# Kernel tuning notes

Measured on AMD Instinct MI355X. Metric: run time of the kernel, lower is better.

The kernel has to match this reference:

```python
import jax, jax.numpy as jnp
import numpy as np

# Model constants (match init_kwargs)
H, P, N, G, NL, K = 32, 64, 128, 1, 15, 4   # heads, head_dim, state, groups, lambda levels, conv width
HID, T, BATCH = 1024, 1024, 1
INTER = H * P                    # 2048
CONV_DIM = INTER + 2 * G * N     # 2304
PROJ = INTER + CONV_DIM + H * (NL + 1)  # 4864
EPS = 1e-5


def _level_matrix(t_len: int) -> np.ndarray:
    """Fenwick-tree level assignment: for query t, prefix [0,t] splits into
    power-of-two segments from binary expansion of t+1; segment of length 2^l -> level l."""
    lm = np.zeros((t_len, t_len), dtype=np.int32)
    for t in range(t_len):
        n = t + 1
        while n > 0:
            lb = n & (-n)
            lm[t, n - lb:n] = lb.bit_length() - 1
            n -= lb
    return lm


def setup_inputs() -> dict:
    key = jax.random.key(0)
    ks = jax.random.split(key, 4)
    return {
        "hidden_states": jax.random.normal(ks[0], (BATCH, T, HID), jnp.float32),
        "in_proj_w": jax.random.normal(ks[1], (PROJ, HID), jnp.float32) / np.sqrt(HID).astype(np.float32),
        "in_proj_b": jnp.zeros((PROJ,), jnp.float32),
        "conv_w": jax.random.normal(ks[2], (CONV_DIM, K), jnp.float32) / np.sqrt(K).astype(np.float32),
        "dt_bias": jnp.ones((H,), jnp.float32),
        "A_log": jnp.log(jnp.arange(1, H + 1, dtype=jnp.float32)),
        "L_param": jnp.ones((H, NL), jnp.float32),
        "D": jnp.ones((H,), jnp.float32),
        "rmsnorm_w": jnp.ones((INTER,), jnp.float32),
        "out_proj_w": jax.random.normal(ks[3], (HID, INTER), jnp.float32) / np.sqrt(INTER).astype(np.float32),
        "out_proj_b": jnp.zeros((HID,), jnp.float32),
        "level_mat": jnp.asarray(_level_matrix(T)),  # (T,T) int32, data-independent
    }


def reference(hidden_states, in_proj_w, in_proj_b, conv_w, dt_bias, A_log,
              L_param, D, rmsnorm_w, out_proj_w, out_proj_b, level_mat):
    b, t, _ = hidden_states.shape
    # in_proj and split: [z | xBC | dt | dl]
    zxbcdtdl = hidden_states @ in_proj_w.T + in_proj_b
    z, xBC, dt, dl = jnp.split(zxbcdtdl, [INTER, INTER + CONV_DIM, INTER + CONV_DIM + H], axis=-1)
    # depthwise causal conv1d (width K) + SiLU
    xp = jnp.pad(xBC, ((0, 0), (K - 1, 0), (0, 0)))
    conv = sum(xp[:, w:w + t, :] * conv_w[:, w] for w in range(K))
    xBC = jax.nn.silu(conv)
    x, Bm, Cm = jnp.split(xBC, [INTER, INTER + G * N], axis=-1)
    x = x.reshape(b, t, H, P)          # v pre-scale
    Bm = Bm.reshape(b, t, G, N)        # keys
    Cm = Cm.reshape(b, t, G, N)        # queries
    dl = dl.reshape(b, t, H, NL)
    # D residual uses unscaled x (matches hmamba_chunk_scan_combined ordering)
    D_res = x * D[None, None, :, None]
    dt = jax.nn.softplus(dt + dt_bias)            # (b,t,H)
    v = x * dt[..., None]                          # (b,t,H,P)
    A = -jnp.exp(A_log)                            # (H,)
    g = A * dt                                     # (b,t,H), per-token log-decay (<=0)
    Ls = jax.nn.softplus(L_param * dl)             # (b,t,H,NL) per-token level scales
    # cumulative log-decay; decay(t,s) = exp(cg_t - cg_s), s<=t
    cg = jnp.cumsum(g, axis=1).transpose(0, 2, 1)  # (b,H,t)
    mask = jnp.tril(jnp.ones((t, t), bool))
    logdecay = jnp.where(mask, cg[:, :, :, None] - cg[:, :, None, :], -jnp.inf)
    decay = jnp.exp(logdecay)                      # (b,H,t,s)
    # hierarchical level scale H[t,s] = Ls[b,t,h, level(t,s)]
    Hmat = jnp.take_along_axis(Ls.transpose(0, 2, 1, 3), level_mat[None, None, :, :], axis=-1)  # (b,H,t,s)
    scores = jnp.einsum('btgn,bsgn->bgts', Cm, Bm)  # (b,G,t,s), G=1 broadcasts over heads
    att = scores * decay * Hmat                     # (b,H,t,s), masked via decay=0
    y = jnp.einsum('bhts,bshp->bthp', att, v) + D_res
    y = y.reshape(b, t, INTER)
    # gated RMSNorm with norm_before_gate=False: normalize(y * silu(z)) * w
    yg = y * jax.nn.silu(z)
    y = yg * jax.lax.rsqrt(jnp.mean(yg * yg, axis=-1, keepdims=True) + EPS) * rmsnorm_w
    return y @ out_proj_w.T + out_proj_b
```

## Files before the change

kernel.cpp:

```cpp
#include <hip/hip_runtime.h>
#include <hip/hip_bf16.h>
#include <math.h>

#define T_LEN 1024
#define HID 1024
#define NHEAD 32
#define HDIM 64
#define NSTATE 128
#define NLVL 15
#define KCONV 4
#define INTER 2048
#define CONV_DIM 2304
#define PROJ 4864
#define EPS 1e-5f

typedef __attribute__((ext_vector_type(8))) _Float16 half8;
typedef __attribute__((ext_vector_type(4))) float float4v;
typedef unsigned short ushort_t;

__device__ __forceinline__ float softplus_f(float x) {
  return fmaxf(x, 0.f) + log1pf(expf(-fabsf(x)));
}
__device__ __forceinline__ float silu_f(float x) {
  return x / (1.f + expf(-x));
}
__device__ __forceinline__ ushort_t f2h(float f) {
  union { _Float16 h; ushort_t u; } v;
  v.h = (_Float16)f;
  return v.u;
}
__device__ __forceinline__ void gload_lds16(const void* g, void* l) {
  __builtin_amdgcn_global_load_lds(
      (const __attribute__((address_space(1))) void*)g,
      (__attribute__((address_space(3))) void*)l, 16, 0, 0);
}

#define N4_HS  (T_LEN * HID / 4)
#define N4_WI  (PROJ * HID / 4)
#define N4_WO  (HID * INTER / 4)
__global__ __launch_bounds__(256) void prep_f16(
    const float* __restrict__ hs, const float* __restrict__ wi,
    const float* __restrict__ wo, ushort_t* __restrict__ hsb,
    ushort_t* __restrict__ wib, ushort_t* __restrict__ wob) {
  int i = blockIdx.x * 256 + threadIdx.x;
  const float* src; ushort_t* dst; int j;
  if (i < N4_HS)              { src = hs; dst = hsb; j = i; }
  else if (i < N4_HS + N4_WI) { src = wi; dst = wib; j = i - N4_HS; }
  else                        { src = wo; dst = wob; j = i - N4_HS - N4_WI; }
  float4 v = reinterpret_cast<const float4*>(src)[j];
  union { ushort_t u[4]; unsigned long long ll; } o;
  o.u[0] = f2h(v.x); o.u[1] = f2h(v.y); o.u[2] = f2h(v.z); o.u[3] = f2h(v.w);
  reinterpret_cast<unsigned long long*>(dst)[j] = o.ll;
}

__global__ __launch_bounds__(256) void gemm_f16_sk(
    const ushort_t* __restrict__ A, const ushort_t* __restrict__ B,
    float* __restrict__ Cpart, int M, int N, int K, int Kc) {
  __shared__ ushort_t As[2][128][32];
  __shared__ ushort_t Bs[2][128][32];
  const int tid = threadIdx.x;
  const int w = tid >> 6, L = tid & 63;
  const int n0 = blockIdx.x * 128, m0 = blockIdx.y * 128;
  const int kbeg = blockIdx.z * Kc;
  float* __restrict__ C = Cpart + (size_t)blockIdx.z * M * N;
  const int mq = (w & 1) * 64, nq = (w >> 1) * 64;
  const int srow = (L >> 2);
  const int sch = (L & 3) * 8;

  float4v acc[4][4];
#pragma unroll
  for (int i = 0; i < 4; ++i)
#pragma unroll
    for (int j = 0; j < 4; ++j) acc[i][j] = (float4v){0.f, 0.f, 0.f, 0.f};

  const int niter = Kc / 32;
  {
    const int kk = kbeg;
#pragma unroll
    for (int j = 0; j < 2; ++j) {
      int r0 = 16 * (w * 2 + j);
      gload_lds16(A + (size_t)(m0 + r0 + srow) * K + kk + sch, &As[0][r0][0]);
      gload_lds16(B + (size_t)(n0 + r0 + srow) * K + kk + sch, &Bs[0][r0][0]);
    }
  }
  for (int it = 0; it < niter; ++it) {
    __syncthreads();
    if (it + 1 < niter) {
      const int kk = kbeg + (it + 1) * 32;
      const int nb = (it + 1) & 1;
#pragma unroll
      for (int j = 0; j < 2; ++j) {
        int r0 = 16 * (w * 2 + j);
        gload_lds16(A + (size_t)(m0 + r0 + srow) * K + kk + sch, &As[nb][r0][0]);
        gload_lds16(B + (size_t)(n0 + r0 + srow) * K + kk + sch, &Bs[nb][r0][0]);
      }
    }
    const int cb = it & 1;
    half8 af[4], bf[4];
#pragma unroll
    for (int t = 0; t < 4; ++t) {
      af[t] = *reinterpret_cast<const half8*>(&As[cb][mq + t * 16 + (L & 15)][(L >> 4) * 8]);
      bf[t] = *reinterpret_cast<const half8*>(&Bs[cb][nq + t * 16 + (L & 15)][(L >> 4) * 8]);
    }
#pragma unroll
    for (int mt = 0; mt < 4; ++mt)
#pragma unroll
      for (int nt = 0; nt < 4; ++nt)
        acc[mt][nt] = __builtin_amdgcn_mfma_f32_16x16x32_f16(af[mt], bf[nt], acc[mt][nt], 0, 0, 0);
  }
  const int qrow = (L >> 4) * 4;
#pragma unroll
  for (int mt = 0; mt < 4; ++mt) {
#pragma unroll
    for (int nt = 0; nt < 4; ++nt) {
      int col = n0 + nq + nt * 16 + (L & 15);
#pragma unroll
      for (int r = 0; r < 4; ++r) {
        int row = m0 + mq + mt * 16 + qrow + r;
        C[(size_t)row * N + col] = acc[mt][nt][r];
      }
    }
  }
}

__global__ __launch_bounds__(256) void reduce_out4(const float* __restrict__ p,
                                                   const float* __restrict__ bias,
                                                   float* __restrict__ out, int MN) {
  int i = blockIdx.x * 256 + threadIdx.x;
  if (i * 4 >= MN) return;
  float4 a = reinterpret_cast<const float4*>(p)[i];
  float4 b = reinterpret_cast<const float4*>(p + MN)[i];
  float4 c = reinterpret_cast<const float4*>(p + 2 * (size_t)MN)[i];
  float4 d = reinterpret_cast<const float4*>(p + 3 * (size_t)MN)[i];
  int col = (i * 4) & (HID - 1);
  float4 bv = *reinterpret_cast<const float4*>(bias + col);
  float4 o;
  o.x = a.x + b.x + c.x + d.x + bv.x;
  o.y = a.y + b.y + c.y + d.y + bv.y;
  o.z = a.z + b.z + c.z + d.z + bv.z;
  o.w = a.w + b.w + c.w + d.w + bv.w;
  reinterpret_cast<float4*>(out)[i] = o;
}

__global__ __launch_bounds__(512) void pointwise_dt(
    const float* __restrict__ zx0, const float* __restrict__ zx1,
    const float* __restrict__ in_b, const float* __restrict__ dt_bias,
    const float* __restrict__ A_log, const float* __restrict__ L_param,
    float* __restrict__ dtbuf, float* __restrict__ gT,
    float* __restrict__ Lsbuf) {
  const int t = blockIdx.x;
  const int j = threadIdx.x;
  const size_t ro = (size_t)t * PROJ;
  if (j < NHEAD * NLVL) {
    int c = INTER + CONV_DIM + NHEAD + j;
    float x = L_param[j] * (zx0[ro + c] + zx1[ro + c] + in_b[c]);
    Lsbuf[(size_t)t * (NHEAD * NLVL) + j] = softplus_f(x);
  } else {
    int h = j - NHEAD * NLVL;
    int c = INTER + CONV_DIM + h;
    float x = zx0[ro + c] + zx1[ro + c] + in_b[c] + dt_bias[h];
    float dt = softplus_f(x);
    dtbuf[t * NHEAD + h] = dt;
    gT[h * T_LEN + t] = -expf(A_log[h]) * dt;
  }
}

__global__ __launch_bounds__(64) void scan_g(const float* __restrict__ gT,
                                             double* __restrict__ cgd) {
  const int h = blockIdx.x, l = threadIdx.x;
  const float* gr = gT + (size_t)h * T_LEN + l * 16;
  double pre[16];
  double acc = 0.0;
#pragma unroll
  for (int i = 0; i < 16; ++i) { acc += (double)gr[i]; pre[i] = acc; }
  double s = acc;
#pragma unroll
  for (int off = 1; off < 64; off <<= 1) {
    double o = __shfl_up(s, off, 64);
    if (l >= off) s += o;
  }
  const double base = s - acc;
  double* cr = cgd + (size_t)h * T_LEN + l * 16;
#pragma unroll
  for (int i = 0; i < 16; ++i) cr[i] = base + pre[i];
}

__global__ __launch_bounds__(256) void conv_fused(
    const float* __restrict__ zx0, const float* __restrict__ zx1,
    const float* __restrict__ in_b, const float* __restrict__ conv_w,
    const float* __restrict__ dtbuf, const float* __restrict__ Dp,
    ushort_t* __restrict__ vt, float* __restrict__ ybuf,
    ushort_t* __restrict__ Bb, ushort_t* __restrict__ Cb) {
  __shared__ ushort_t Vl[64][68];
  __shared__ float dtl[64];
  const int tq = blockIdx.x, cy = blockIdx.y;
  const int t0 = tq * 64;
  const int tid = threadIdx.x;
  const int lane = tid & 63, g = tid >> 6;
  const bool vpath = (cy < 32);
  const int ccol = vpath ? cy * 64 + lane : INTER + (cy - 32) * 64 + lane;
  const int zcol = INTER + ccol;
  float cw[KCONV];
#pragma unroll
  for (int w = 0; w < KCONV; ++w) cw[w] = conv_w[ccol * KCONV + w];
  const float bc = in_b[zcol];
  if (vpath && tid < 64) dtl[tid] = dtbuf[(t0 + tid) * NHEAD + cy];
  const float Dh = vpath ? Dp[cy] : 0.f;

  float xv[19];
#pragma unroll
  for (int i = 0; i < 19; ++i) {
    int tt = t0 + g * 16 - 3 + i;
    if (tt >= 0) {
      size_t o = (size_t)tt * PROJ + zcol;
      xv[i] = zx0[o] + zx1[o] + bc;
    } else xv[i] = 0.f;
  }
  __syncthreads();
#pragma unroll
  for (int i = 0; i < 16; ++i) {
    float acc = xv[i] * cw[0] + xv[i + 1] * cw[1] + xv[i + 2] * cw[2] + xv[i + 3] * cw[3];
    float sil = silu_f(acc);
    int tl = g * 16 + i;
    int t = t0 + tl;
    if (vpath) {
      ushort_t vh = f2h(sil * dtl[tl]);
      Vl[tl][lane] = vh;
      ybuf[(size_t)t * INTER + cy * 64 + lane] = sil * Dh;
    } else if (ccol < INTER + NSTATE) {
      Bb[t * NSTATE + (ccol - INTER)] = f2h(sil);
    } else {
      Cb[t * NSTATE + (ccol - INTER - NSTATE)] = f2h(sil);
    }
  }
  if (vpath) {
    __syncthreads();
#pragma unroll
    for (int rep = 0; rep < 2; ++rep) {
      int u = tid + 256 * rep;
      int p = u >> 3, t8 = (u & 7) * 8;
      union { ushort_t u16[8]; half8 h; } o;
#pragma unroll
      for (int j = 0; j < 8; ++j) o.u16[j] = Vl[t8 + j][p];
      *reinterpret_cast<half8*>(vt + (size_t)(cy * 64 + p) * T_LEN + t0 + t8) = o.h;
    }
  }
}

__global__ __launch_bounds__(256) void attn_mfma(
    const ushort_t* __restrict__ Bb, const ushort_t* __restrict__ Cb,
    const ushort_t* __restrict__ vt, const double* __restrict__ cgd,
    const float* __restrict__ Lsb, float* __restrict__ ybuf) {
  __shared__ ushort_t Bl[64][136];
  __shared__ ushort_t Vtl[64][72];
  __shared__ ushort_t Sl[64][72];
  __shared__ float Lsl[64][16];
  __shared__ float cgq[64];
  __shared__ float cgs[64];

  const int item = blockIdx.x;
  const int h = item / 40;
  const int rem = item - h * 40;
  int qt, j;
  if (rem < 4)        { qt = rem;                 j = 0; }
  else if (rem < 12)  { qt = 4 + (rem - 4) / 2;   j = (rem - 4) % 2; }
  else if (rem < 24)  { qt = 8 + (rem - 12) / 3;  j = (rem - 12) % 3; }
  else                { qt = 12 + (rem - 24) / 4; j = (rem - 24) % 4; }

  const int tid = threadIdx.x;
  const int w = tid >> 6, L = tid & 63;
  const int tq0 = qt * 64;
  const double* cgh = cgd + (size_t)h * T_LEN;
  const double base = cgh[tq0];

  for (int i = tid; i < 64 * NLVL; i += 256) {
    int r = i / NLVL, l = i - r * NLVL;
    Lsl[r][l] = Lsb[(size_t)(tq0 + r) * (NHEAD * NLVL) + h * NLVL + l];
  }
  if (tid < 64) cgq[tid] = (float)(cgh[tq0 + tid] - base);

  half8 cfrag[4];
  {
    const ushort_t* cr = Cb + (size_t)(tq0 + w * 16 + (L & 15)) * NSTATE + (L >> 4) * 8;
#pragma unroll
    for (int ks = 0; ks < 4; ++ks)
      cfrag[ks] = *reinterpret_cast<const half8*>(cr + ks * 32);
  }
  float4v yac[4];
#pragma unroll
  for (int i = 0; i < 4; ++i) yac[i] = (float4v){0.f, 0.f, 0.f, 0.f};

  const int qrow = w * 16 + ((L >> 4) << 2);

  const int st0 = 4 * j;
  const int st1 = min(4 * j + 4, qt + 1);
  for (int st = st0; st < st1; ++st) {
    const int ts0 = st * 64;
    __syncthreads();
#pragma unroll
    for (int i = 0; i < 4; ++i) {
      int u = tid + 256 * i;
      int row = u >> 4, kb = (u & 15) * 8;
      *reinterpret_cast<half8*>(&Bl[row][kb]) =
          *reinterpret_cast<const half8*>(Bb + (size_t)(ts0 + row) * NSTATE + kb);
    }
#pragma unroll
    for (int i = 0; i < 2; ++i) {
      int u = tid + 256 * i;
      int p = u >> 3, sc = (u & 7) * 8;
      *reinterpret_cast<half8*>(&Vtl[p][sc]) =
          *reinterpret_cast<const half8*>(vt + (size_t)(h * HDIM + p) * T_LEN + ts0 + sc);
    }
    if (tid < 64) cgs[tid] = (float)(cgh[ts0 + tid] - base);
    __syncthreads();

    float4v sac[4];
#pragma unroll
    for (int nt = 0; nt < 4; ++nt) sac[nt] = (float4v){0.f, 0.f, 0.f, 0.f};
#pragma unroll
    for (int ks = 0; ks < 4; ++ks) {
#pragma unroll
      for (int nt = 0; nt < 4; ++nt) {
        half8 bfrag = *reinterpret_cast<const half8*>(&Bl[nt * 16 + (L & 15)][ks * 32 + (L >> 4) * 8]);
        sac[nt] = __builtin_amdgcn_mfma_f32_16x16x32_f16(cfrag[ks], bfrag, sac[nt], 0, 0, 0);
      }
    }
#pragma unroll
    for (int nt = 0; nt < 4; ++nt) {
      int s = nt * 16 + (L & 15);
      int sg = ts0 + s;
      float cs = cgs[s];
#pragma unroll
      for (int r = 0; r < 4; ++r) {
        int q = qrow + r;
        int tg = tq0 + q;
        float val = 0.f;
        if (sg <= tg) {
          int lvl = 31 - __clz((unsigned)(sg ^ (tg + 1)));
          val = sac[nt][r] * __expf(cgq[q] - cs) * Lsl[q][lvl];
        }
        Sl[q][s] = f2h(val);
      }
    }
    __builtin_amdgcn_s_waitcnt(0);
#pragma unroll
    for (int ks = 0; ks < 2; ++ks) {
      half8 af = *reinterpret_cast<const half8*>(&Sl[w * 16 + (L & 15)][ks * 32 + (L >> 4) * 8]);
#pragma unroll
      for (int pt = 0; pt < 4; ++pt) {
        half8 bfv = *reinterpret_cast<const half8*>(&Vtl[pt * 16 + (L & 15)][ks * 32 + (L >> 4) * 8]);
        yac[pt] = __builtin_amdgcn_mfma_f32_16x16x32_f16(af, bfv, yac[pt], 0, 0, 0);
      }
    }
  }
#pragma unroll
  for (int pt = 0; pt < 4; ++pt) {
    int p = pt * 16 + (L & 15);
#pragma unroll
    for (int r = 0; r < 4; ++r) {
      int q = qrow + r;
      atomicAdd(ybuf + (size_t)(tq0 + q) * INTER + h * HDIM + p, yac[pt][r]);
    }
  }
}

__global__ __launch_bounds__(256) void rmsnorm_gate(
    const float* __restrict__ ybuf, const float* __restrict__ zx0,
    const float* __restrict__ zx1, const float* __restrict__ in_b,
    const float* __restrict__ w, ushort_t* __restrict__ yhf) {
  __shared__ float red[4];
  const int t = blockIdx.x, tid = threadIdx.x;
  const size_t ro = (size_t)t * PROJ;
  const float* yrow = ybuf + (size_t)t * INTER;
  float yg[8];
  float ss = 0.f;
#pragma unroll
  for (int i = 0; i < 8; ++i) {
    int c = tid + 256 * i;
    float z = zx0[ro + c] + zx1[ro + c] + in_b[c];
    float g = yrow[c] * silu_f(z);
    yg[i] = g;
    ss += g * g;
  }
#pragma unroll
  for (int off = 32; off; off >>= 1) ss += __shfl_down(ss, off, 64);
  if ((tid & 63) == 0) red[tid >> 6] = ss;
  __syncthreads();
  if (tid == 0) red[0] = red[0] + red[1] + red[2] + red[3];
  __syncthreads();
  const float scale = rsqrtf(red[0] / (float)INTER + EPS);
#pragma unroll
  for (int i = 0; i < 8; ++i) {
    int c = tid + 256 * i;
    yhf[(size_t)t * INTER + c] = f2h(yg[i] * scale * w[c]);
  }
}

extern "C" void kernel_launch(void* const* d_in, const int* in_sizes, int n_in,
                              void* d_out, int out_size, void* d_ws, size_t ws_size,
                              hipStream_t stream) {
  const float* hs        = (const float*)d_in[0];
  const float* in_proj_w = (const float*)d_in[1];
  const float* in_proj_b = (const float*)d_in[2];
  const float* conv_w    = (const float*)d_in[3];
  const float* dt_bias   = (const float*)d_in[4];
  const float* A_log     = (const float*)d_in[5];
  const float* L_param   = (const float*)d_in[6];
  const float* Dp        = (const float*)d_in[7];
  const float* rms_w     = (const float*)d_in[8];
  const float* out_proj_w= (const float*)d_in[9];
  const float* out_proj_b= (const float*)d_in[10];
  float* out = (float*)d_out;

  char* W = (char*)d_ws;
  size_t off = 0;
  auto alloc = [&](size_t bytes) { void* p = W + off; off = (off + bytes + 255) & ~(size_t)255; return p; };
  double*   cgd = (double*)  alloc((size_t)NHEAD * T_LEN * 8);
  float*    zx0 = (float*)   alloc((size_t)T_LEN * PROJ * 4);
  float*    zx1 = (float*)   alloc((size_t)T_LEN * PROJ * 4);
  float*    opp = (float*)   alloc((size_t)4 * T_LEN * HID * 4);
  float*    ybuf= (float*)   alloc((size_t)T_LEN * INTER * 4);
  float*    gT  = (float*)   alloc((size_t)NHEAD * T_LEN * 4);
  float*    dtb = (float*)   alloc((size_t)T_LEN * NHEAD * 4);
  float*    Lsb = (float*)   alloc((size_t)T_LEN * NHEAD * NLVL * 4);
  ushort_t* hsb = (ushort_t*)alloc((size_t)T_LEN * HID * 2);
  ushort_t* Wib = (ushort_t*)alloc((size_t)PROJ * HID * 2);
  ushort_t* Wob = (ushort_t*)alloc((size_t)HID * INTER * 2);
  ushort_t* yhf = (ushort_t*)alloc((size_t)T_LEN * INTER * 2);
  ushort_t* vt  = (ushort_t*)alloc((size_t)T_LEN * INTER * 2);
  ushort_t* Bb  = (ushort_t*)alloc((size_t)T_LEN * NSTATE * 2);
  ushort_t* Cb  = (ushort_t*)alloc((size_t)T_LEN * NSTATE * 2);

  prep_f16<<<(N4_HS + N4_WI + N4_WO) / 256, 256, 0, stream>>>(
      hs, in_proj_w, out_proj_w, hsb, Wib, Wob);

  gemm_f16_sk<<<dim3(PROJ / 128, T_LEN / 128, 2), 256, 0, stream>>>(
      hsb, Wib, zx0, T_LEN, PROJ, HID, HID / 2);

  pointwise_dt<<<T_LEN, 512, 0, stream>>>(zx0, zx1, in_proj_b, dt_bias, A_log, L_param,
                                          dtb, gT, Lsb);

  scan_g<<<NHEAD, 64, 0, stream>>>(gT, cgd);

  conv_fused<<<dim3(T_LEN / 64, 36), 256, 0, stream>>>(
      zx0, zx1, in_proj_b, conv_w, dtb, Dp, vt, ybuf, Bb, Cb);

  attn_mfma<<<NHEAD * 40, 256, 0, stream>>>(Bb, Cb, vt, cgd, Lsb, ybuf);

  rmsnorm_gate<<<T_LEN, 256, 0, stream>>>(ybuf, zx0, zx1, in_proj_b, rms_w, yhf);

  gemm_f16_sk<<<dim3(HID / 128, T_LEN / 128, 4), 256, 0, stream>>>(
      yhf, Wob, opp, T_LEN, HID, INTER, INTER / 4);
  reduce_out4<<<(T_LEN * HID / 4 + 255) / 256, 256, 0, stream>>>(
      opp, out_proj_b, out, T_LEN * HID);
}
```

Baseline: 200.2 us.

## Store split-K GEMM partials in fp16 and fuse dt/level pointwise into consumers

The split-K GEMM now writes its partial sums as fp16 instead of fp32, which halves the traffic for the in_proj and out_proj intermediates that every later stage reads. The separate pointwise_dt kernel is removed. dt softplus and the decay product move into scan_g, and the per-level softplus is recomputed inside the attention kernel, which cuts a launch and the gT/Ls buffers. It also relaxes one waitcnt in the attention loop. Storing partial sums in fp16 loses precision before the reduction and may raise the numerical error.

After: 200.7 us. About the same (+0.2%).

```diff
diff --git a/kernel.cpp b/kernel.cpp
--- a/kernel.cpp
+++ b/kernel.cpp
@@ -28,6 +28,11 @@
   union { _Float16 h; ushort_t u; } v;
   v.h = (_Float16)f;
   return v.u;
+}
+__device__ __forceinline__ float h2f(ushort_t u) {
+  union { ushort_t u; _Float16 h; } v;
+  v.u = u;
+  return (float)v.h;
 }
 __device__ __forceinline__ void gload_lds16(const void* g, void* l) {
   __builtin_amdgcn_global_load_lds(
@@ -55,14 +60,14 @@
 
 __global__ __launch_bounds__(256) void gemm_f16_sk(
     const ushort_t* __restrict__ A, const ushort_t* __restrict__ B,
-    float* __restrict__ Cpart, int M, int N, int K, int Kc) {
+    ushort_t* __restrict__ Cpart, int M, int N, int K, int Kc) {
   __shared__ ushort_t As[2][128][32];
   __shared__ ushort_t Bs[2][128][32];
   const int tid = threadIdx.x;
   const int w = tid >> 6, L = tid & 63;
   const int n0 = blockIdx.x * 128, m0 = blockIdx.y * 128;
   const int kbeg = blockIdx.z * Kc;
-  float* __restrict__ C = Cpart + (size_t)blockIdx.z * M * N;
+  ushort_t* __restrict__ C = Cpart + (size_t)blockIdx.z * M * N;
   const int mq = (w & 1) * 64, nq = (w >> 1) * 64;
   const int srow = (L >> 2);
   const int sch = (L & 3) * 8;
@@ -117,62 +122,52 @@
 #pragma unroll
       for (int r = 0; r < 4; ++r) {
         int row = m0 + mq + mt * 16 + qrow + r;
-        C[(size_t)row * N + col] = acc[mt][nt][r];
+        C[(size_t)row * N + col] = f2h(acc[mt][nt][r]);
       }
     }
   }
 }
 
-__global__ __launch_bounds__(256) void reduce_out4(const float* __restrict__ p,
+__global__ __launch_bounds__(256) void reduce_out4(const ushort_t* __restrict__ p,
                                                    const float* __restrict__ bias,
                                                    float* __restrict__ out, int MN) {
   int i = blockIdx.x * 256 + threadIdx.x;
-  if (i * 4 >= MN) return;
-  float4 a = reinterpret_cast<const float4*>(p)[i];
-  float4 b = reinterpret_cast<const float4*>(p + MN)[i];
-  float4 c = reinterpret_cast<const float4*>(p + 2 * (size_t)MN)[i];
-  float4 d = reinterpret_cast<const float4*>(p + 3 * (size_t)MN)[i];
-  int col = (i * 4) & (HID - 1);
-  float4 bv = *reinterpret_cast<const float4*>(bias + col);
-  float4 o;
-  o.x = a.x + b.x + c.x + d.x + bv.x;
-  o.y = a.y + b.y + c.y + d.y + bv.y;
-  o.z = a.z + b.z + c.z + d.z + bv.z;
-  o.w = a.w + b.w + c.w + d.w + bv.w;
-  reinterpret_cast<float4*>(out)[i] = o;
-}
-
-__global__ __launch_bounds__(512) void pointwise_dt(
-    const float* __restrict__ zx0, const float* __restrict__ zx1,
+  if (i * 8 >= MN) return;
+  half8 a = reinterpret_cast<const half8*>(p)[i];
+  half8 b = reinterpret_cast<const half8*>(p + MN)[i];
+  half8 c = reinterpret_cast<const half8*>(p + 2 * (size_t)MN)[i];
+  half8 d = reinterpret_cast<const half8*>(p + 3 * (size_t)MN)[i];
+  int col = (i * 8) & (HID - 1);
+  float o[8];
+#pragma unroll
+  for (int j = 0; j < 8; ++j)
+    o[j] = (float)a[j] + (float)b[j] + (float)c[j] + (float)d[j] + bias[col + j];
+  float4 o0 = {o[0], o[1], o[2], o[3]}, o1 = {o[4], o[5], o[6], o[7]};
+  reinterpret_cast<float4*>(out)[i * 2] = o0;
+  reinterpret_cast<float4*>(out)[i * 2 + 1] = o1;
+}
+
+__global__ __launch_bounds__(64) void scan_g(
+    const ushort_t* __restrict__ zh0, const ushort_t* __restrict__ zh1,
     const float* __restrict__ in_b, const float* __restrict__ dt_bias,
-    const float* __restrict__ A_log, const float* __restrict__ L_param,
-    float* __restrict__ dtbuf, float* __restrict__ gT,
-    float* __restrict__ Lsbuf) {
-  const int t = blockIdx.x;
-  const int j = threadIdx.x;
-  const size_t ro = (size_t)t * PROJ;
-  if (j < NHEAD * NLVL) {
-    int c = INTER + CONV_DIM + NHEAD + j;
-    float x = L_param[j] * (zx0[ro + c] + zx1[ro + c] + in_b[c]);
-    Lsbuf[(size_t)t * (NHEAD * NLVL) + j] = softplus_f(x);
-  } else {
-    int h = j - NHEAD * NLVL;
-    int c = INTER + CONV_DIM + h;
-    float x = zx0[ro + c] + zx1[ro + c] + in_b[c] + dt_bias[h];
-    float dt = softplus_f(x);
-    dtbuf[t * NHEAD + h] = dt;
-    gT[h * T_LEN + t] = -expf(A_log[h]) * dt;
-  }
-}
-
-__global__ __launch_bounds__(64) void scan_g(const float* __restrict__ gT,
-                                             double* __restrict__ cgd) {
+    const float* __restrict__ A_log, float* __restrict__ dtb,
+    double* __restrict__ cgd) {
   const int h = blockIdx.x, l = threadIdx.x;
-  const float* gr = gT + (size_t)h * T_LEN + l * 16;
+  const int c = INTER + CONV_DIM + h;
+  const float bb = in_b[c] + dt_bias[h];
+  const float Ae = -expf(A_log[h]);
   double pre[16];
   double acc = 0.0;
 #pragma unroll
-  for (int i = 0; i < 16; ++i) { acc += (double)gr[i]; pre[i] = acc; }
+  for (int i = 0; i < 16; ++i) {
+    int t = l * 16 + i;
+    size_t o = (size_t)t * PROJ + c;
+    float x = h2f(zh0[o]) + h2f(zh1[o]) + bb;
+    float dt = softplus_f(x);
+    dtb[t * NHEAD + h] = dt;
+    acc += (double)(Ae * dt);
+    pre[i] = acc;
+  }
   double s = acc;
 #pragma unroll
   for (int off = 1; off < 64; off <<= 1) {
@@ -186,9 +181,9 @@
 }
 
 __global__ __launch_bounds__(256) void conv_fused(
-    const float* __restrict__ zx0, const float* __restrict__ zx1,
+    const ushort_t* __restrict__ zh0, const ushort_t* __restrict__ zh1,
     const float* __restrict__ in_b, const float* __restrict__ conv_w,
-    const float* __restrict__ dtbuf, const float* __restrict__ Dp,
+    const float* __restrict__ dtb, const float* __restrict__ Dp,
     ushort_t* __restrict__ vt, float* __restrict__ ybuf,
     ushort_t* __restrict__ Bb, ushort_t* __restrict__ Cb) {
   __shared__ ushort_t Vl[64][68];
@@ -204,7 +199,7 @@
 #pragma unroll
   for (int w = 0; w < KCONV; ++w) cw[w] = conv_w[ccol * KCONV + w];
   const float bc = in_b[zcol];
-  if (vpath && tid < 64) dtl[tid] = dtbuf[(t0 + tid) * NHEAD + cy];
+  if (vpath && tid < 64) dtl[tid] = dtb[(t0 + tid) * NHEAD + cy];
   const float Dh = vpath ? Dp[cy] : 0.f;
 
   float xv[19];
@@ -213,7 +208,7 @@
     int tt = t0 + g * 16 - 3 + i;
     if (tt >= 0) {
       size_t o = (size_t)tt * PROJ + zcol;
-      xv[i] = zx0[o] + zx1[o] + bc;
+      xv[i] = h2f(zh0[o]) + h2f(zh1[o]) + bc;
     } else xv[i] = 0.f;
   }
   __syncthreads();
@@ -224,8 +219,7 @@
     int tl = g * 16 + i;
     int t = t0 + tl;
     if (vpath) {
-      ushort_t vh = f2h(sil * dtl[tl]);
-      Vl[tl][lane] = vh;
+      Vl[tl][lane] = f2h(sil * dtl[tl]);
       ybuf[(size_t)t * INTER + cy * 64 + lane] = sil * Dh;
     } else if (ccol < INTER + NSTATE) {
       Bb[t * NSTATE + (ccol - INTER)] = f2h(sil);
@@ -250,7 +244,9 @@
 __global__ __launch_bounds__(256) void attn_mfma(
     const ushort_t* __restrict__ Bb, const ushort_t* __restrict__ Cb,
     const ushort_t* __restrict__ vt, const double* __restrict__ cgd,
-    const float* __restrict__ Lsb, float* __restrict__ ybuf) {
+    const ushort_t* __restrict__ zh0, const ushort_t* __restrict__ zh1,
+    const float* __restrict__ in_b, const float* __restrict__ L_param,
+    float* __restrict__ ybuf) {
   __shared__ ushort_t Bl[64][136];
   __shared__ ushort_t Vtl[64][72];
   __shared__ ushort_t Sl[64][72];
@@ -275,7 +271,10 @@
 
   for (int i = tid; i < 64 * NLVL; i += 256) {
     int r = i / NLVL, l = i - r * NLVL;
-    Lsl[r][l] = Lsb[(size_t)(tq0 + r) * (NHEAD * NLVL) + h * NLVL + l];
+    int cc = INTER + CONV_DIM + NHEAD + h * NLVL + l;
+    size_t o = (size_t)(tq0 + r) * PROJ + cc;
+    float x = h2f(zh0[o]) + h2f(zh1[o]) + in_b[cc];
+    Lsl[r][l] = softplus_f(L_param[h * NLVL + l] * x);
   }
   if (tid < 64) cgq[tid] = (float)(cgh[tq0 + tid] - base);
 
@@ -342,7 +341,7 @@
         Sl[q][s] = f2h(val);
       }
     }
-    __builtin_amdgcn_s_waitcnt(0);
+    __builtin_amdgcn_s_waitcnt(0xC07F);
 #pragma unroll
     for (int ks = 0; ks < 2; ++ks) {
       half8 af = *reinterpret_cast<const half8*>(&Sl[w * 16 + (L & 15)][ks * 32 + (L >> 4) * 8]);
@@ -365,8 +364,8 @@
 }
 
 __global__ __launch_bounds__(256) void rmsnorm_gate(
-    const float* __restrict__ ybuf, const float* __restrict__ zx0,
-    const float* __restrict__ zx1, const float* __restrict__ in_b,
+    const float* __restrict__ ybuf, const ushort_t* __restrict__ zh0,
+    const ushort_t* __restrict__ zh1, const float* __restrict__ in_b,
     const float* __restrict__ w, ushort_t* __restrict__ yhf) {
   __shared__ float red[4];
   const int t = blockIdx.x, tid = threadIdx.x;
@@ -377,7 +376,7 @@
 #pragma unroll
   for (int i = 0; i < 8; ++i) {
     int c = tid + 256 * i;
-    float z = zx0[ro + c] + zx1[ro + c] + in_b[c];
+    float z = h2f(zh0[ro + c]) + h2f(zh1[ro + c]) + in_b[c];
     float g = yrow[c] * silu_f(z);
     yg[i] = g;
     ss += g * g;
@@ -416,13 +415,10 @@
   size_t off = 0;
   auto alloc = [&](size_t bytes) { void* p = W + off; off = (off + bytes + 255) & ~(size_t)255; return p; };
   double*   cgd = (double*)  alloc((size_t)NHEAD * T_LEN * 8);
-  float*    zx0 = (float*)   alloc((size_t)T_LEN * PROJ * 4);
-  float*    zx1 = (float*)   alloc((size_t)T_LEN * PROJ * 4);
-  float*    opp = (float*)   alloc((size_t)4 * T_LEN * HID * 4);
+  ushort_t* zh  = (ushort_t*)alloc((size_t)2 * T_LEN * PROJ * 2);
+  ushort_t* opp = (ushort_t*)alloc((size_t)4 * T_LEN * HID * 2);
   float*    ybuf= (float*)   alloc((size_t)T_LEN * INTER * 4);
-  float*    gT  = (float*)   alloc((size_t)NHEAD * T_LEN * 4);
   float*    dtb = (float*)   alloc((size_t)T_LEN * NHEAD * 4);
-  float*    Lsb = (float*)   alloc((size_t)T_LEN * NHEAD * NLVL * 4);
   ushort_t* hsb = (ushort_t*)alloc((size_t)T_LEN * HID * 2);
   ushort_t* Wib = (ushort_t*)alloc((size_t)PROJ * HID * 2);
   ushort_t* Wob = (ushort_t*)alloc((size_t)HID * INTER * 2);
@@ -430,27 +426,27 @@
   ushort_t* vt  = (ushort_t*)alloc((size_t)T_LEN * INTER * 2);
   ushort_t* Bb  = (ushort_t*)alloc((size_t)T_LEN * NSTATE * 2);
   ushort_t* Cb  = (ushort_t*)alloc((size_t)T_LEN * NSTATE * 2);
+  ushort_t* zh0 = zh;
+  ushort_t* zh1 = zh + (size_t)T_LEN * PROJ;
 
   prep_f16<<<(N4_HS + N4_WI + N4_WO) / 256, 256, 0, stream>>>(
       hs, in_proj_w, out_proj_w, hsb, Wib, Wob);
 
   gemm_f16_sk<<<dim3(PROJ / 128, T_LEN / 128, 2), 256, 0, stream>>>(
-      hsb, Wib, zx0, T_LEN, PROJ, HID, HID / 2);
-
-  pointwise_dt<<<T_LEN, 512, 0, stream>>>(zx0, zx1, in_proj_b, dt_bias, A_log, L_param,
-                                          dtb, gT, Lsb);
-
-  scan_g<<<NHEAD, 64, 0, stream>>>(gT, cgd);
+      hsb, Wib, zh, T_LEN, PROJ, HID, HID / 2);
+
+  scan_g<<<NHEAD, 64, 0, stream>>>(zh0, zh1, in_proj_b, dt_bias, A_log, dtb, cgd);
 
   conv_fused<<<dim3(T_LEN / 64, 36), 256, 0, stream>>>(
-      zx0, zx1, in_proj_b, conv_w, dtb, Dp, vt, ybuf, Bb, Cb);
-
-  attn_mfma<<<NHEAD * 40, 256, 0, stream>>>(Bb, Cb, vt, cgd, Lsb, ybuf);
-
-  rmsnorm_gate<<<T_LEN, 256, 0, stream>>>(ybuf, zx0, zx1, in_proj_b, rms_w, yhf);
+      zh0, zh1, in_proj_b, conv_w, dtb, Dp, vt, ybuf, Bb, Cb);
+
+  attn_mfma<<<NHEAD * 40, 256, 0, stream>>>(Bb, Cb, vt, cgd, zh0, zh1, in_proj_b,
+                                            L_param, ybuf);
+
+  rmsnorm_gate<<<T_LEN, 256, 0, stream>>>(ybuf, zh0, zh1, in_proj_b, rms_w, yhf);
 
   gemm_f16_sk<<<dim3(HID / 128, T_LEN / 128, 4), 256, 0, stream>>>(
       yhf, Wob, opp, T_LEN, HID, INTER, INTER / 4);
-  reduce_out4<<<(T_LEN * HID / 4 + 255) / 256, 256, 0, stream>>>(
+  reduce_out4<<<(T_LEN * HID / 8 + 255) / 256, 256, 0, stream>>>(
       opp, out_proj_b, out, T_LEN * HID);
 }
```
